# Kernel optimization log

Measured on AMD Instinct MI355X. Metric: run time of the kernel, lower is better.

## Reference

```python
import jax, jax.numpy as jnp
import numpy as np

EMBED_DIM = 1024
HEADS = 16
HEAD_DIM = EMBED_DIM // HEADS


def setup_inputs() -> dict:
    key = jax.random.key(0)
    ks = jax.random.split(key, 9)
    D = EMBED_DIM
    s = 1.0 / np.sqrt(D)
    x = jax.random.normal(ks[0], (4, 2048, D), dtype=jnp.float32)
    Wq = jax.random.uniform(ks[1], (D, D), jnp.float32, -s, s)
    bq = jnp.zeros((D,), jnp.float32)
    Wk = jax.random.uniform(ks[2], (D, D), jnp.float32, -s, s)
    bk = jnp.zeros((D,), jnp.float32)
    Wv = jax.random.uniform(ks[3], (D, D), jnp.float32, -s, s)
    bv = jnp.zeros((D,), jnp.float32)
    Wo = jax.random.uniform(ks[4], (D, D), jnp.float32, -s, s)
    bo = jnp.zeros((D,), jnp.float32)
    gamma = jnp.ones((D,), jnp.float32)
    beta = jnp.zeros((D,), jnp.float32)
    return {"x": x, "Wq": Wq, "bq": bq, "Wk": Wk, "bk": bk,
            "Wv": Wv, "bv": bv, "Wo": Wo, "bo": bo,
            "gamma": gamma, "beta": beta}


def reference(x, Wq, bq, Wk, bk, Wv, bv, Wo, bo, gamma, beta):
    B, S, D = x.shape
    H, Dh = HEADS, HEAD_DIM
    # projections -> [B, H, S, Dh]
    q = (x @ Wq + bq).reshape(B, S, H, Dh).transpose(0, 2, 1, 3)
    k = (x @ Wk + bk).reshape(B, S, H, Dh).transpose(0, 2, 1, 3)
    v = (x @ Wv + bv).reshape(B, S, H, Dh).transpose(0, 2, 1, 3)
    scores = jnp.einsum('bhqd,bhkd->bhqk', q, k) / jnp.sqrt(jnp.float32(Dh))
    attn = jax.nn.softmax(scores, axis=-1)  # dropout is identity in eval
    ctx = jnp.einsum('bhqk,bhkd->bhqd', attn, v)
    ctx = ctx.transpose(0, 2, 1, 3).reshape(B, S, D)
    out = ctx @ Wo + bo
    # residual + LayerNorm (eps=1e-5, torch default)
    h = out + x
    mu = jnp.mean(h, axis=-1, keepdims=True)
    var = jnp.mean(jnp.square(h - mu), axis=-1, keepdims=True)
    return (h - mu) * jax.lax.rsqrt(var + 1e-5) * gamma + beta
```

## Files before the change

kernel.cpp:

```cpp
#include <hip/hip_runtime.h>
#include <hip/hip_bf16.h>
#include <stdint.h>

typedef short sh4 __attribute__((ext_vector_type(4)));
typedef short sh8 __attribute__((ext_vector_type(8)));
typedef float fl4 __attribute__((ext_vector_type(4)));
typedef float f32x4 __attribute__((ext_vector_type(4)));
typedef float f32x16 __attribute__((ext_vector_type(16)));
typedef uint32_t u32x4 __attribute__((ext_vector_type(4)));

static __device__ __forceinline__ short f2bf(float f) {
  union { float f; uint32_t u; } v;
  v.f = f;
  uint32_t r = v.u + 0x7fffu + ((v.u >> 16) & 1u);
  return (short)(r >> 16);
}

static __device__ __forceinline__ uint32_t cvt_pk_bf16(float a, float b) {
  uint32_t r;
  asm("v_cvt_pk_bf16_f32 %0, %1, %2" : "=v"(r) : "v"(a), "v"(b));
  return r;
}

static __device__ __forceinline__ void pl32swap(uint32_t& a, uint32_t& b) {
  asm volatile("v_permlane32_swap_b32 %0, %1" : "+v"(a), "+v"(b));
}

static __device__ __forceinline__ void gload_lds16(const void* g, void* l) {
  __builtin_amdgcn_global_load_lds((const __attribute__((address_space(1))) void*)g,
                                   (__attribute__((address_space(3))) void*)l, 16, 0, 0);
}

__global__ __launch_bounds__(256) void k_wt(const float* __restrict__ Wq, const float* __restrict__ Wk,
                                            const float* __restrict__ Wv, const float* __restrict__ Wo,
                                            short* __restrict__ Tq, short* __restrict__ Tk,
                                            short* __restrict__ Tv, short* __restrict__ To) {
  const float* W = blockIdx.z == 0 ? Wq : blockIdx.z == 1 ? Wk : blockIdx.z == 2 ? Wv : Wo;
  short* T = blockIdx.z == 0 ? Tq : blockIdx.z == 1 ? Tk : blockIdx.z == 2 ? Tv : To;
  __shared__ float tile[32][33];
  int n0 = blockIdx.x * 32, k0 = blockIdx.y * 32;
  int tx = threadIdx.x, ty = threadIdx.y;
#pragma unroll
  for (int p = 0; p < 4; p++) tile[ty + 8 * p][tx] = W[(size_t)(k0 + ty + 8 * p) * 1024 + n0 + tx];
  __syncthreads();
#pragma unroll
  for (int p = 0; p < 4; p++) T[(size_t)(n0 + ty + 8 * p) * 1024 + k0 + tx] = f2bf(tile[tx][ty + 8 * p]);
}

__global__ __launch_bounds__(256) void k_cvtx(const float* __restrict__ x, short* __restrict__ o) {
  int i = blockIdx.x * 256 + threadIdx.x;
  fl4 v = ((const fl4*)x)[i];
  sh4 r;
#pragma unroll
  for (int j = 0; j < 4; j++) r[j] = f2bf(v[j]);
  ((sh4*)o)[i] = r;
}

#define GEMM_PIPE_LOOP(STAGE_BODY, COMPUTE_BODY)                         \
  STAGE_BODY(0, 0);                                                      \
  STAGE_BODY(1, 1);                                                      \
  {                                                                      \
    int bufc = 0, bufs = 2;                                              \
    for (int it = 0; it < 32; it++) {                                    \
      if (it < 31)                                                       \
        asm volatile("s_waitcnt vmcnt(4)" ::: "memory");                 \
      else                                                               \
        asm volatile("s_waitcnt vmcnt(0)" ::: "memory");                 \
      __builtin_amdgcn_s_barrier();                                      \
      if (it + 2 < 32) { STAGE_BODY(it + 2, bufs); }                     \
      __builtin_amdgcn_sched_barrier(0);                                 \
      { int buf = bufc; COMPUTE_BODY }                                   \
      bufc = bufc == 2 ? 0 : bufc + 1;                                   \
      bufs = bufs == 2 ? 0 : bufs + 1;                                   \
      asm volatile("" ::: "memory");                                     \
    }                                                                    \
  }

__global__ __launch_bounds__(256) void k_qk(const short* __restrict__ A, const short* __restrict__ WT2,
                                            const float* __restrict__ bq, const float* __restrict__ bk,
                                            short* __restrict__ Qo, short* __restrict__ Ko, float qscale) {
  __shared__ __align__(16) short As[3][128 * 32];
  __shared__ __align__(16) short Bs[3][128 * 32];
  const int xcd = blockIdx.x & 7, j = blockIdx.x >> 3;
  const int m0 = (xcd + 8 * (j & 7)) * 128, n0 = (j >> 3) * 128;
  const int sec = n0 >> 10;
  const float* bias = sec == 0 ? bq : bk;
  short* Out = sec == 0 ? Qo : Ko;
  const float scale = sec == 0 ? qscale : 1.f;
  const int t = threadIdx.x;
  const int lane = t & 63, w = t >> 6;
  const int wr = w >> 1, wc = w & 1;
  const int l15 = lane & 15, g = lane >> 4;
  f32x4 acc[4][4];
#pragma unroll
  for (int mi = 0; mi < 4; mi++)
#pragma unroll
    for (int ni = 0; ni < 4; ni++) acc[mi][ni] = (f32x4){0.f, 0.f, 0.f, 0.f};

#define QK_STAGE(kt, buf)                                                                     \
  {                                                                                           \
    int r0 = w * 32;                                                                          \
    _Pragma("unroll") for (int i = 0; i < 2; i++) {                                           \
      int row = r0 + i * 16 + (lane >> 2);                                                    \
      gload_lds16(&A[(size_t)(m0 + row) * 1024 + (kt) * 32 + (lane & 3) * 8],                 \
                  &As[buf][(r0 + i * 16) * 32]);                                              \
      gload_lds16(&WT2[(size_t)(n0 + row) * 1024 + (kt) * 32 + (lane & 3) * 8],               \
                  &Bs[buf][(r0 + i * 16) * 32]);                                              \
    }                                                                                         \
  }

#define QK_COMPUTE                                                                            \
  sh8 a[4], b[4];                                                                             \
  _Pragma("unroll") for (int i = 0; i < 4; i++)                                               \
      a[i] = *(sh8*)&As[buf][(wr * 64 + i * 16 + l15) * 32 + g * 8];                          \
  _Pragma("unroll") for (int i = 0; i < 4; i++)                                               \
      b[i] = *(sh8*)&Bs[buf][(wc * 64 + i * 16 + l15) * 32 + g * 8];                          \
  _Pragma("unroll") for (int mi = 0; mi < 4; mi++)                                            \
      _Pragma("unroll") for (int ni = 0; ni < 4; ni++)                                        \
          acc[mi][ni] = __builtin_amdgcn_mfma_f32_16x16x32_bf16(b[ni], a[mi], acc[mi][ni], 0, 0, 0);

  GEMM_PIPE_LOOP(QK_STAGE, QK_COMPUTE)

#pragma unroll
  for (int ni = 0; ni < 4; ni++) {
    int nbase = n0 + wc * 64 + ni * 16 + g * 4;
    int nn0 = nbase & 1023;
    fl4 bv4 = *(const fl4*)&bias[nn0];
    int h = nn0 >> 6, dh0 = nn0 & 63;
#pragma unroll
    for (int mi = 0; mi < 4; mi++) {
      int m = m0 + wr * 64 + mi * 16 + l15;
      int bb = m >> 11, s = m & 2047;
      uint2 dd;
      dd.x = cvt_pk_bf16((acc[mi][ni][0] + bv4[0]) * scale, (acc[mi][ni][1] + bv4[1]) * scale);
      dd.y = cvt_pk_bf16((acc[mi][ni][2] + bv4[2]) * scale, (acc[mi][ni][3] + bv4[3]) * scale);
      *(uint2*)&Out[(((size_t)bb * 16 + h) * 2048 + s) * 64 + dh0] = dd;
    }
  }
}

__global__ __launch_bounds__(256) void k_v(const short* __restrict__ A, const short* __restrict__ WTv,
                                           const float* __restrict__ bv, short* __restrict__ Vo) {
  __shared__ __align__(16) short As[3][128 * 32];
  __shared__ __align__(16) short Bs[3][128 * 32];
  const int xcd = blockIdx.x & 7, j = blockIdx.x >> 3;
  const int m0 = (xcd + 8 * (j & 7)) * 128, n0 = (j >> 3) * 128;
  const int t = threadIdx.x;
  const int lane = t & 63, w = t >> 6;
  const int wr = w >> 1, wc = w & 1;
  const int l15 = lane & 15, g = lane >> 4;
  f32x4 acc[4][4];
#pragma unroll
  for (int mi = 0; mi < 4; mi++)
#pragma unroll
    for (int ni = 0; ni < 4; ni++) acc[mi][ni] = (f32x4){0.f, 0.f, 0.f, 0.f};

#define V_STAGE(kt, buf)                                                                      \
  {                                                                                           \
    int r0 = w * 32;                                                                          \
    _Pragma("unroll") for (int i = 0; i < 2; i++) {                                           \
      int row = r0 + i * 16 + (lane >> 2);                                                    \
      gload_lds16(&A[(size_t)(m0 + row) * 1024 + (kt) * 32 + (lane & 3) * 8],                 \
                  &As[buf][(r0 + i * 16) * 32]);                                              \
      gload_lds16(&WTv[(size_t)(n0 + row) * 1024 + (kt) * 32 + (lane & 3) * 8],               \
                  &Bs[buf][(r0 + i * 16) * 32]);                                              \
    }                                                                                         \
  }

#define V_COMPUTE                                                                             \
  sh8 a[4], b[4];                                                                             \
  _Pragma("unroll") for (int i = 0; i < 4; i++)                                               \
      a[i] = *(sh8*)&As[buf][(wr * 64 + i * 16 + l15) * 32 + g * 8];                          \
  _Pragma("unroll") for (int i = 0; i < 4; i++)                                               \
      b[i] = *(sh8*)&Bs[buf][(wc * 64 + i * 16 + l15) * 32 + g * 8];                          \
  _Pragma("unroll") for (int mi = 0; mi < 4; mi++)                                            \
      _Pragma("unroll") for (int ni = 0; ni < 4; ni++)                                        \
          acc[mi][ni] = __builtin_amdgcn_mfma_f32_16x16x32_bf16(a[mi], b[ni], acc[mi][ni], 0, 0, 0);

  GEMM_PIPE_LOOP(V_STAGE, V_COMPUTE)

#pragma unroll
  for (int ni = 0; ni < 4; ni++) {
    int col = n0 + wc * 64 + ni * 16 + l15;
    int nn = col & 1023;
    float bvv = bv[nn];
    int h = nn >> 6, dh = nn & 63;
#pragma unroll
    for (int mi = 0; mi < 4; mi++) {
      int mr = m0 + wr * 64 + mi * 16 + g * 4;
      int bb = mr >> 11, s = mr & 2047;
      uint2 dd;
      dd.x = cvt_pk_bf16(acc[mi][ni][0] + bvv, acc[mi][ni][1] + bvv);
      dd.y = cvt_pk_bf16(acc[mi][ni][2] + bvv, acc[mi][ni][3] + bvv);
      *(uint2*)&Vo[(((size_t)bb * 16 + h) * 64 + dh) * 2048 + s] = dd;
    }
  }
}

__global__ __launch_bounds__(256) void k_oproj(const short* __restrict__ A, const short* __restrict__ BT,
                                               const float* __restrict__ bias, const float* __restrict__ X,
                                               float* __restrict__ Out) {
  __shared__ __align__(16) short As[3][128 * 32];
  __shared__ __align__(16) short Bs[3][128 * 32];
  const int xcd = blockIdx.x & 7, j = blockIdx.x >> 3;
  const int m0 = (xcd + 8 * (j & 7)) * 128, n0 = (j >> 3) * 128;
  const int t = threadIdx.x;
  const int lane = t & 63, w = t >> 6;
  const int wr = w >> 1, wc = w & 1;
  const int l15 = lane & 15, g = lane >> 4;
  f32x4 acc[4][4];
#pragma unroll
  for (int mi = 0; mi < 4; mi++)
#pragma unroll
    for (int ni = 0; ni < 4; ni++) acc[mi][ni] = (f32x4){0.f, 0.f, 0.f, 0.f};

#define O_STAGE(kt, buf)                                                                      \
  {                                                                                           \
    int r0 = w * 32;                                                                          \
    _Pragma("unroll") for (int i = 0; i < 2; i++) {                                           \
      int row = r0 + i * 16 + (lane >> 2);                                                    \
      gload_lds16(&A[(size_t)(m0 + row) * 1024 + (kt) * 32 + (lane & 3) * 8],                 \
                  &As[buf][(r0 + i * 16) * 32]);                                              \
      gload_lds16(&BT[(size_t)(n0 + row) * 1024 + (kt) * 32 + (lane & 3) * 8],                \
                  &Bs[buf][(r0 + i * 16) * 32]);                                              \
    }                                                                                         \
  }

#define O_COMPUTE                                                                             \
  sh8 a[4], b[4];                                                                             \
  _Pragma("unroll") for (int i = 0; i < 4; i++)                                               \
      a[i] = *(sh8*)&As[buf][(wr * 64 + i * 16 + l15) * 32 + g * 8];                          \
  _Pragma("unroll") for (int i = 0; i < 4; i++)                                               \
      b[i] = *(sh8*)&Bs[buf][(wc * 64 + i * 16 + l15) * 32 + g * 8];                          \
  _Pragma("unroll") for (int mi = 0; mi < 4; mi++)                                            \
      _Pragma("unroll") for (int ni = 0; ni < 4; ni++)                                        \
          acc[mi][ni] = __builtin_amdgcn_mfma_f32_16x16x32_bf16(b[ni], a[mi], acc[mi][ni], 0, 0, 0);

  GEMM_PIPE_LOOP(O_STAGE, O_COMPUTE)

#pragma unroll
  for (int ni = 0; ni < 4; ni++) {
    int nbase = n0 + wc * 64 + ni * 16 + g * 4;
    fl4 bv4 = *(const fl4*)&bias[nbase];
#pragma unroll
    for (int mi = 0; mi < 4; mi++) {
      int m = m0 + wr * 64 + mi * 16 + l15;
      fl4 xv = *(const fl4*)&X[(size_t)m * 1024 + nbase];
      fl4 r;
#pragma unroll
      for (int e = 0; e < 4; e++) r[e] = acc[mi][ni][e] + bv4[e] + xv[e];
      *(fl4*)&Out[(size_t)m * 1024 + nbase] = r;
    }
  }
}

__global__ __launch_bounds__(512, 4) void k_attn(const short* __restrict__ Q, const short* __restrict__ K,
                                                 const short* __restrict__ Vt, short* __restrict__ CTX) {
  const int nid = (blockIdx.x & 7) * 64 + (blockIdx.x >> 3);
  const int qbi = nid & 7, h = (nid >> 3) & 15, b = nid >> 7;
  const int q0 = qbi * 256;
  const size_t ho = (((size_t)b * 16 + h) * 2048) * 64;
  const short* Qh = Q + ho;
  const short* Kh = K + ho;
  const short* Vh = Vt + ho;
  __shared__ __align__(16) short Ks[3][8 * 512];
  __shared__ __align__(16) short Vs[4][8 * 512];
  const int t = threadIdx.x, lane = t & 63, w = t >> 6;
  const int l31 = lane & 31, hi = lane >> 5;

  sh8 qreg[4];
#pragma unroll
  for (int ks = 0; ks < 4; ks++)
    qreg[ks] = *(const sh8*)&Qh[(size_t)(q0 + w * 32 + l31) * 64 + ks * 16 + hi * 8];

  f32x16 zinit;
#pragma unroll
  for (int r = 0; r < 16; r++) zinit[r] = 0.f;

  f32x16 oc0 = zinit, oc1 = zinit;
  float l_s = 0.f;
  u32x4 pwp[4];

  auto stageK = [&](int kt, int buf) {
    gload_lds16(&Kh[(size_t)(kt * 64 + (w >> 2) * 32 + l31) * 64 + (w & 3) * 16 + hi * 8],
                (char*)&Ks[buf][0] + w * 1024);
  };
  auto stageV = [&](int kt, int buf) {
    gload_lds16(&Vh[(size_t)((w >> 2) * 32 + l31) * 2048 + kt * 64 + (w & 3) * 16 + hi * 8],
                (char*)&Vs[buf][0] + w * 1024);
  };

  stageK(0, 0); stageV(0, 0);
  stageK(1, 1); stageV(1, 1);

  for (int kt = 0; kt < 32; kt++) {
    if (kt < 31)
      asm volatile("s_waitcnt vmcnt(2)" ::: "memory");
    else
      asm volatile("s_waitcnt vmcnt(0)" ::: "memory");
    __builtin_amdgcn_s_barrier();
    if (kt + 2 < 32) { stageK(kt + 2, (kt + 2) % 3); stageV(kt + 2, (kt + 2) & 3); }
    __builtin_amdgcn_sched_barrier(0);
    const int kbuf = kt % 3;

    f32x16 s0, s1;
    __builtin_amdgcn_s_setprio(1);
#pragma unroll
    for (int ks = 0; ks < 4; ks++) {
      sh8 ak0 = *(sh8*)((char*)&Ks[kbuf][0] + ks * 1024 + lane * 16);
      sh8 ak1 = *(sh8*)((char*)&Ks[kbuf][0] + (4 + ks) * 1024 + lane * 16);
      if (ks == 0) {
        s0 = __builtin_amdgcn_mfma_f32_32x32x16_bf16(ak0, qreg[0], zinit, 0, 0, 0);
        s1 = __builtin_amdgcn_mfma_f32_32x32x16_bf16(ak1, qreg[0], zinit, 0, 0, 0);
      } else {
        s0 = __builtin_amdgcn_mfma_f32_32x32x16_bf16(ak0, qreg[ks], s0, 0, 0, 0);
        s1 = __builtin_amdgcn_mfma_f32_32x32x16_bf16(ak1, qreg[ks], s1, 0, 0, 0);
      }
    }

    if (kt > 0) {
      const int vb = (kt - 1) & 3;
#pragma unroll
      for (int ks = 0; ks < 4; ks++) {
        sh8 pb = __builtin_bit_cast(sh8, pwp[ks]);
        sh8 av0 = *(sh8*)((char*)&Vs[vb][0] + ks * 1024 + lane * 16);
        sh8 av1 = *(sh8*)((char*)&Vs[vb][0] + (4 + ks) * 1024 + lane * 16);
        oc0 = __builtin_amdgcn_mfma_f32_32x32x16_bf16(av0, pb, oc0, 0, 0, 0);
        oc1 = __builtin_amdgcn_mfma_f32_32x32x16_bf16(av1, pb, oc1, 0, 0, 0);
      }
    }
    __builtin_amdgcn_s_setprio(0);

    float ps = 0.f;
#pragma unroll
    for (int r = 0; r < 16; r++) { s0[r] = __builtin_amdgcn_exp2f(s0[r]); ps += s0[r]; }
#pragma unroll
    for (int r = 0; r < 16; r++) { s1[r] = __builtin_amdgcn_exp2f(s1[r]); ps += s1[r]; }
    l_s += ps;

    {
      uint32_t a0 = cvt_pk_bf16(s0[0], s0[1]), a1 = cvt_pk_bf16(s0[2], s0[3]);
      uint32_t b0 = cvt_pk_bf16(s0[4], s0[5]), b1 = cvt_pk_bf16(s0[6], s0[7]);
      uint32_t c0 = cvt_pk_bf16(s0[8], s0[9]), c1 = cvt_pk_bf16(s0[10], s0[11]);
      uint32_t d0 = cvt_pk_bf16(s0[12], s0[13]), d1 = cvt_pk_bf16(s0[14], s0[15]);
      pl32swap(a0, b0); pl32swap(a1, b1); pl32swap(c0, d0); pl32swap(c1, d1);
      pwp[0] = (u32x4){a0, a1, b0, b1};
      pwp[1] = (u32x4){c0, c1, d0, d1};
      a0 = cvt_pk_bf16(s1[0], s1[1]); a1 = cvt_pk_bf16(s1[2], s1[3]);
      b0 = cvt_pk_bf16(s1[4], s1[5]); b1 = cvt_pk_bf16(s1[6], s1[7]);
      c0 = cvt_pk_bf16(s1[8], s1[9]); c1 = cvt_pk_bf16(s1[10], s1[11]);
      d0 = cvt_pk_bf16(s1[12], s1[13]); d1 = cvt_pk_bf16(s1[14], s1[15]);
      pl32swap(a0, b0); pl32swap(a1, b1); pl32swap(c0, d0); pl32swap(c1, d1);
      pwp[2] = (u32x4){a0, a1, b0, b1};
      pwp[3] = (u32x4){c0, c1, d0, d1};
    }
    asm volatile("" ::: "memory");
  }

  {
    const int vb = 31 & 3;
    __builtin_amdgcn_s_setprio(1);
#pragma unroll
    for (int ks = 0; ks < 4; ks++) {
      sh8 pb = __builtin_bit_cast(sh8, pwp[ks]);
      sh8 av0 = *(sh8*)((char*)&Vs[vb][0] + ks * 1024 + lane * 16);
      sh8 av1 = *(sh8*)((char*)&Vs[vb][0] + (4 + ks) * 1024 + lane * 16);
      oc0 = __builtin_amdgcn_mfma_f32_32x32x16_bf16(av0, pb, oc0, 0, 0, 0);
      oc1 = __builtin_amdgcn_mfma_f32_32x32x16_bf16(av1, pb, oc1, 0, 0, 0);
    }
    __builtin_amdgcn_s_setprio(0);
  }

  l_s += __shfl_xor(l_s, 32);
  float li = 1.f / l_s;
  int s = q0 + w * 32 + l31;
  size_t obase = (((size_t)b * 2048 + s) * 16 + h) * 64;
#pragma unroll
  for (int rq = 0; rq < 4; rq++) {
    uint2 dd;
    dd.x = cvt_pk_bf16(oc0[4 * rq] * li, oc0[4 * rq + 1] * li);
    dd.y = cvt_pk_bf16(oc0[4 * rq + 2] * li, oc0[4 * rq + 3] * li);
    *(uint2*)&CTX[obase + rq * 8 + hi * 4] = dd;
    dd.x = cvt_pk_bf16(oc1[4 * rq] * li, oc1[4 * rq + 1] * li);
    dd.y = cvt_pk_bf16(oc1[4 * rq + 2] * li, oc1[4 * rq + 3] * li);
    *(uint2*)&CTX[obase + 32 + rq * 8 + hi * 4] = dd;
  }
}

__global__ __launch_bounds__(256) void k_ln(float* __restrict__ Out, const float* __restrict__ gamma,
                                            const float* __restrict__ beta) {
  int row = blockIdx.x * 4 + (threadIdx.x >> 6);
  int lane = threadIdx.x & 63;
  float* p = Out + (size_t)row * 1024;
  fl4 v[4];
  float s = 0.f, s2 = 0.f;
#pragma unroll
  for (int j = 0; j < 4; j++) {
    v[j] = *(fl4*)&p[lane * 4 + j * 256];
#pragma unroll
    for (int e = 0; e < 4; e++) { s += v[j][e]; s2 += v[j][e] * v[j][e]; }
  }
#pragma unroll
  for (int off = 1; off < 64; off <<= 1) {
    s += __shfl_xor(s, off);
    s2 += __shfl_xor(s2, off);
  }
  float mu = s * (1.f / 1024.f);
  float var = s2 * (1.f / 1024.f) - mu * mu;
  float inv = rsqrtf(var + 1e-5f);
#pragma unroll
  for (int j = 0; j < 4; j++) {
    fl4 r;
#pragma unroll
    for (int e = 0; e < 4; e++) {
      int c = lane * 4 + j * 256 + e;
      r[e] = (v[j][e] - mu) * inv * gamma[c] + beta[c];
    }
    *(fl4*)&p[lane * 4 + j * 256] = r;
  }
}

extern "C" void kernel_launch(void* const* d_in, const int* in_sizes, int n_in,
                              void* d_out, int out_size, void* d_ws, size_t ws_size,
                              hipStream_t stream) {
  (void)in_sizes; (void)n_in; (void)out_size; (void)ws_size;
  const float* x = (const float*)d_in[0];
  const float* Wq = (const float*)d_in[1];
  const float* bq = (const float*)d_in[2];
  const float* Wk = (const float*)d_in[3];
  const float* bk = (const float*)d_in[4];
  const float* Wv = (const float*)d_in[5];
  const float* bv = (const float*)d_in[6];
  const float* Wo = (const float*)d_in[7];
  const float* bo = (const float*)d_in[8];
  const float* gamma = (const float*)d_in[9];
  const float* beta = (const float*)d_in[10];
  float* out = (float*)d_out;
  char* ws = (char*)d_ws;
  short* xbf = (short*)(ws);
  short* wtq = (short*)(ws + (16ull << 20));
  short* wtk = (short*)(ws + (18ull << 20));
  short* wtv = (short*)(ws + (20ull << 20));
  short* wto = (short*)(ws + (22ull << 20));
  short* qb  = (short*)(ws + (24ull << 20));
  short* kbuf = (short*)(ws + (40ull << 20));
  short* vbuf = (short*)(ws + (56ull << 20));
  short* ctx = (short*)(ws + (72ull << 20));

  const float QSCALE = 0.125f * 1.44269504088896f;

  k_wt<<<dim3(32, 32, 4), dim3(32, 8), 0, stream>>>(Wq, Wk, Wv, Wo, wtq, wtk, wtv, wto);
  k_cvtx<<<8192, 256, 0, stream>>>(x, xbf);
  k_qk<<<1024, 256, 0, stream>>>(xbf, wtq, bq, bk, qb, kbuf, QSCALE);
  k_v<<<512, 256, 0, stream>>>(xbf, wtv, bv, vbuf);
  k_attn<<<512, 512, 0, stream>>>(qb, kbuf, vbuf, ctx);
  k_oproj<<<512, 256, 0, stream>>>(ctx, wto, bo, x, out);
  k_ln<<<2048, 256, 0, stream>>>(out, gamma, beta);
}
```

Measured before the change: 212.9 us.

## Switch projection GEMMs to 32x32x16 MFMA with fragment-ordered LDS layout and new tiling

All three projection GEMMs (QK, V, O) move from 16x16x32 to 32x32x16 bf16 MFMA. Global-to-LDS loads are rearranged so each 1KB LDS chunk already holds one MFMA operand fragment, letting each lane read its fragment with a single contiguous 16-byte load. The QK kernel grows to 256x128 tiles with 512 threads, and the block-to-tile mappings are reassigned so blocks on the same XCD share weight columns for L2 reuse. The intent is fewer LDS instructions and bank conflicts per MFMA and better cache locality, at the cost of higher register pressure from the larger accumulators and changed occupancy hints.

```diff
diff --git a/kernel.cpp b/kernel.cpp
--- a/kernel.cpp
+++ b/kernel.cpp
@@ -56,14 +56,14 @@
   ((sh4*)o)[i] = r;
 }
 
-#define GEMM_PIPE_LOOP(STAGE_BODY, COMPUTE_BODY)                         \
+#define PIPE_LOOP(STAGE_BODY, COMPUTE_BODY, VM)                          \
   STAGE_BODY(0, 0);                                                      \
   STAGE_BODY(1, 1);                                                      \
   {                                                                      \
     int bufc = 0, bufs = 2;                                              \
     for (int it = 0; it < 32; it++) {                                    \
       if (it < 31)                                                       \
-        asm volatile("s_waitcnt vmcnt(4)" ::: "memory");                 \
+        asm volatile("s_waitcnt vmcnt(" VM ")" ::: "memory");            \
       else                                                               \
         asm volatile("s_waitcnt vmcnt(0)" ::: "memory");                 \
       __builtin_amdgcn_s_barrier();                                      \
@@ -76,13 +76,13 @@
     }                                                                    \
   }
 
-__global__ __launch_bounds__(256) void k_qk(const short* __restrict__ A, const short* __restrict__ WT2,
-                                            const float* __restrict__ bq, const float* __restrict__ bk,
-                                            short* __restrict__ Qo, short* __restrict__ Ko, float qscale) {
-  __shared__ __align__(16) short As[3][128 * 32];
-  __shared__ __align__(16) short Bs[3][128 * 32];
+__global__ __launch_bounds__(512, 4) void k_qk(const short* __restrict__ A, const short* __restrict__ WT2,
+                                               const float* __restrict__ bq, const float* __restrict__ bk,
+                                               short* __restrict__ Qo, short* __restrict__ Ko, float qscale) {
+  __shared__ __align__(16) short As[3][8192];
+  __shared__ __align__(16) short Bs[3][4096];
   const int xcd = blockIdx.x & 7, j = blockIdx.x >> 3;
-  const int m0 = (xcd + 8 * (j & 7)) * 128, n0 = (j >> 3) * 128;
+  const int m0 = (j >> 1) * 256, n0 = (xcd * 2 + (j & 1)) * 128;
   const int sec = n0 >> 10;
   const float* bias = sec == 0 ? bq : bk;
   short* Out = sec == 0 ? Qo : Ko;
@@ -90,166 +90,186 @@
   const int t = threadIdx.x;
   const int lane = t & 63, w = t >> 6;
   const int wr = w >> 1, wc = w & 1;
-  const int l15 = lane & 15, g = lane >> 4;
-  f32x4 acc[4][4];
-#pragma unroll
-  for (int mi = 0; mi < 4; mi++)
-#pragma unroll
-    for (int ni = 0; ni < 4; ni++) acc[mi][ni] = (f32x4){0.f, 0.f, 0.f, 0.f};
+  const int l31 = lane & 31, hi = lane >> 5;
+  f32x16 acc[2][2];
+#pragma unroll
+  for (int mi = 0; mi < 2; mi++)
+#pragma unroll
+    for (int ni = 0; ni < 2; ni++)
+#pragma unroll
+      for (int r = 0; r < 16; r++) acc[mi][ni][r] = 0.f;
 
 #define QK_STAGE(kt, buf)                                                                     \
   {                                                                                           \
-    int r0 = w * 32;                                                                          \
-    _Pragma("unroll") for (int i = 0; i < 2; i++) {                                           \
-      int row = r0 + i * 16 + (lane >> 2);                                                    \
-      gload_lds16(&A[(size_t)(m0 + row) * 1024 + (kt) * 32 + (lane & 3) * 8],                 \
-                  &As[buf][(r0 + i * 16) * 32]);                                              \
-      gload_lds16(&WT2[(size_t)(n0 + row) * 1024 + (kt) * 32 + (lane & 3) * 8],               \
-                  &Bs[buf][(r0 + i * 16) * 32]);                                              \
-    }                                                                                         \
+    _Pragma("unroll") for (int i = 0; i < 2; i++)                                             \
+        gload_lds16(&A[(size_t)(m0 + w * 32 + l31) * 1024 + (kt) * 32 + i * 16 + hi * 8],     \
+                    (char*)&As[buf][0] + (w * 2 + i) * 1024);                                 \
+    gload_lds16(&WT2[(size_t)(n0 + (w >> 1) * 32 + l31) * 1024 + (kt) * 32 + (w & 1) * 16 + hi * 8], \
+                (char*)&Bs[buf][0] + w * 1024);                                               \
   }
 
 #define QK_COMPUTE                                                                            \
-  sh8 a[4], b[4];                                                                             \
-  _Pragma("unroll") for (int i = 0; i < 4; i++)                                               \
-      a[i] = *(sh8*)&As[buf][(wr * 64 + i * 16 + l15) * 32 + g * 8];                          \
-  _Pragma("unroll") for (int i = 0; i < 4; i++)                                               \
-      b[i] = *(sh8*)&Bs[buf][(wc * 64 + i * 16 + l15) * 32 + g * 8];                          \
-  _Pragma("unroll") for (int mi = 0; mi < 4; mi++)                                            \
-      _Pragma("unroll") for (int ni = 0; ni < 4; ni++)                                        \
-          acc[mi][ni] = __builtin_amdgcn_mfma_f32_16x16x32_bf16(b[ni], a[mi], acc[mi][ni], 0, 0, 0);
-
-  GEMM_PIPE_LOOP(QK_STAGE, QK_COMPUTE)
-
-#pragma unroll
-  for (int ni = 0; ni < 4; ni++) {
-    int nbase = n0 + wc * 64 + ni * 16 + g * 4;
-    int nn0 = nbase & 1023;
-    fl4 bv4 = *(const fl4*)&bias[nn0];
-    int h = nn0 >> 6, dh0 = nn0 & 63;
-#pragma unroll
-    for (int mi = 0; mi < 4; mi++) {
-      int m = m0 + wr * 64 + mi * 16 + l15;
-      int bb = m >> 11, s = m & 2047;
-      uint2 dd;
-      dd.x = cvt_pk_bf16((acc[mi][ni][0] + bv4[0]) * scale, (acc[mi][ni][1] + bv4[1]) * scale);
-      dd.y = cvt_pk_bf16((acc[mi][ni][2] + bv4[2]) * scale, (acc[mi][ni][3] + bv4[3]) * scale);
-      *(uint2*)&Out[(((size_t)bb * 16 + h) * 2048 + s) * 64 + dh0] = dd;
-    }
-  }
-}
-
-__global__ __launch_bounds__(256) void k_v(const short* __restrict__ A, const short* __restrict__ WTv,
-                                           const float* __restrict__ bv, short* __restrict__ Vo) {
-  __shared__ __align__(16) short As[3][128 * 32];
-  __shared__ __align__(16) short Bs[3][128 * 32];
+  _Pragma("unroll") for (int ks = 0; ks < 2; ks++) {                                          \
+    sh8 a0 = *(sh8*)((char*)&As[buf][0] + ((2 * wr + 0) * 2 + ks) * 1024 + lane * 16);        \
+    sh8 a1 = *(sh8*)((char*)&As[buf][0] + ((2 * wr + 1) * 2 + ks) * 1024 + lane * 16);        \
+    sh8 b0 = *(sh8*)((char*)&Bs[buf][0] + ((2 * wc + 0) * 2 + ks) * 1024 + lane * 16);        \
+    sh8 b1 = *(sh8*)((char*)&Bs[buf][0] + ((2 * wc + 1) * 2 + ks) * 1024 + lane * 16);        \
+    acc[0][0] = __builtin_amdgcn_mfma_f32_32x32x16_bf16(b0, a0, acc[0][0], 0, 0, 0);          \
+    acc[0][1] = __builtin_amdgcn_mfma_f32_32x32x16_bf16(b1, a0, acc[0][1], 0, 0, 0);          \
+    acc[1][0] = __builtin_amdgcn_mfma_f32_32x32x16_bf16(b0, a1, acc[1][0], 0, 0, 0);          \
+    acc[1][1] = __builtin_amdgcn_mfma_f32_32x32x16_bf16(b1, a1, acc[1][1], 0, 0, 0);          \
+  }
+
+  PIPE_LOOP(QK_STAGE, QK_COMPUTE, "3")
+
+#pragma unroll
+  for (int mi = 0; mi < 2; mi++) {
+    int m = m0 + (2 * wr + mi) * 32 + l31;
+    int bb = m >> 11, s = m & 2047;
+#pragma unroll
+    for (int ni = 0; ni < 2; ni++) {
+      int nbase0 = n0 + (2 * wc + ni) * 32;
+#pragma unroll
+      for (int rq = 0; rq < 4; rq++) {
+        int n_lo = nbase0 + 8 * rq + 4 * hi;
+        int nn = n_lo & 1023;
+        fl4 bv4 = *(const fl4*)&bias[nn];
+        int h = nn >> 6, dh0 = nn & 63;
+        uint2 dd;
+        dd.x = cvt_pk_bf16((acc[mi][ni][4 * rq] + bv4[0]) * scale,
+                           (acc[mi][ni][4 * rq + 1] + bv4[1]) * scale);
+        dd.y = cvt_pk_bf16((acc[mi][ni][4 * rq + 2] + bv4[2]) * scale,
+                           (acc[mi][ni][4 * rq + 3] + bv4[3]) * scale);
+        *(uint2*)&Out[(((size_t)bb * 16 + h) * 2048 + s) * 64 + dh0] = dd;
+      }
+    }
+  }
+}
+
+__global__ __launch_bounds__(256, 3) void k_v(const short* __restrict__ A, const short* __restrict__ WTv,
+                                              const float* __restrict__ bv, short* __restrict__ Vo) {
+  __shared__ __align__(16) short As[3][4096];
+  __shared__ __align__(16) short Bs[3][4096];
   const int xcd = blockIdx.x & 7, j = blockIdx.x >> 3;
-  const int m0 = (xcd + 8 * (j & 7)) * 128, n0 = (j >> 3) * 128;
+  const int m0 = j * 128, n0 = xcd * 128;
   const int t = threadIdx.x;
   const int lane = t & 63, w = t >> 6;
   const int wr = w >> 1, wc = w & 1;
-  const int l15 = lane & 15, g = lane >> 4;
-  f32x4 acc[4][4];
-#pragma unroll
-  for (int mi = 0; mi < 4; mi++)
-#pragma unroll
-    for (int ni = 0; ni < 4; ni++) acc[mi][ni] = (f32x4){0.f, 0.f, 0.f, 0.f};
+  const int l31 = lane & 31, hi = lane >> 5;
+  f32x16 acc[2][2];
+#pragma unroll
+  for (int mi = 0; mi < 2; mi++)
+#pragma unroll
+    for (int ni = 0; ni < 2; ni++)
+#pragma unroll
+      for (int r = 0; r < 16; r++) acc[mi][ni][r] = 0.f;
 
 #define V_STAGE(kt, buf)                                                                      \
   {                                                                                           \
-    int r0 = w * 32;                                                                          \
     _Pragma("unroll") for (int i = 0; i < 2; i++) {                                           \
-      int row = r0 + i * 16 + (lane >> 2);                                                    \
-      gload_lds16(&A[(size_t)(m0 + row) * 1024 + (kt) * 32 + (lane & 3) * 8],                 \
-                  &As[buf][(r0 + i * 16) * 32]);                                              \
-      gload_lds16(&WTv[(size_t)(n0 + row) * 1024 + (kt) * 32 + (lane & 3) * 8],               \
-                  &Bs[buf][(r0 + i * 16) * 32]);                                              \
+      int c = 2 * w + i;                                                                      \
+      gload_lds16(&A[(size_t)(m0 + (c >> 1) * 32 + l31) * 1024 + (kt) * 32 + (c & 1) * 16 + hi * 8], \
+                  (char*)&As[buf][0] + c * 1024);                                             \
+      gload_lds16(&WTv[(size_t)(n0 + (c >> 1) * 32 + l31) * 1024 + (kt) * 32 + (c & 1) * 16 + hi * 8], \
+                  (char*)&Bs[buf][0] + c * 1024);                                             \
     }                                                                                         \
   }
 
 #define V_COMPUTE                                                                             \
-  sh8 a[4], b[4];                                                                             \
-  _Pragma("unroll") for (int i = 0; i < 4; i++)                                               \
-      a[i] = *(sh8*)&As[buf][(wr * 64 + i * 16 + l15) * 32 + g * 8];                          \
-  _Pragma("unroll") for (int i = 0; i < 4; i++)                                               \
-      b[i] = *(sh8*)&Bs[buf][(wc * 64 + i * 16 + l15) * 32 + g * 8];                          \
-  _Pragma("unroll") for (int mi = 0; mi < 4; mi++)                                            \
-      _Pragma("unroll") for (int ni = 0; ni < 4; ni++)                                        \
-          acc[mi][ni] = __builtin_amdgcn_mfma_f32_16x16x32_bf16(a[mi], b[ni], acc[mi][ni], 0, 0, 0);
-
-  GEMM_PIPE_LOOP(V_STAGE, V_COMPUTE)
-
-#pragma unroll
-  for (int ni = 0; ni < 4; ni++) {
-    int col = n0 + wc * 64 + ni * 16 + l15;
-    int nn = col & 1023;
-    float bvv = bv[nn];
-    int h = nn >> 6, dh = nn & 63;
-#pragma unroll
-    for (int mi = 0; mi < 4; mi++) {
-      int mr = m0 + wr * 64 + mi * 16 + g * 4;
-      int bb = mr >> 11, s = mr & 2047;
-      uint2 dd;
-      dd.x = cvt_pk_bf16(acc[mi][ni][0] + bvv, acc[mi][ni][1] + bvv);
-      dd.y = cvt_pk_bf16(acc[mi][ni][2] + bvv, acc[mi][ni][3] + bvv);
-      *(uint2*)&Vo[(((size_t)bb * 16 + h) * 64 + dh) * 2048 + s] = dd;
-    }
-  }
-}
-
-__global__ __launch_bounds__(256) void k_oproj(const short* __restrict__ A, const short* __restrict__ BT,
-                                               const float* __restrict__ bias, const float* __restrict__ X,
-                                               float* __restrict__ Out) {
-  __shared__ __align__(16) short As[3][128 * 32];
-  __shared__ __align__(16) short Bs[3][128 * 32];
+  _Pragma("unroll") for (int ks = 0; ks < 2; ks++) {                                          \
+    sh8 a0 = *(sh8*)((char*)&As[buf][0] + ((2 * wr + 0) * 2 + ks) * 1024 + lane * 16);        \
+    sh8 a1 = *(sh8*)((char*)&As[buf][0] + ((2 * wr + 1) * 2 + ks) * 1024 + lane * 16);        \
+    sh8 b0 = *(sh8*)((char*)&Bs[buf][0] + ((2 * wc + 0) * 2 + ks) * 1024 + lane * 16);        \
+    sh8 b1 = *(sh8*)((char*)&Bs[buf][0] + ((2 * wc + 1) * 2 + ks) * 1024 + lane * 16);        \
+    acc[0][0] = __builtin_amdgcn_mfma_f32_32x32x16_bf16(a0, b0, acc[0][0], 0, 0, 0);          \
+    acc[0][1] = __builtin_amdgcn_mfma_f32_32x32x16_bf16(a0, b1, acc[0][1], 0, 0, 0);          \
+    acc[1][0] = __builtin_amdgcn_mfma_f32_32x32x16_bf16(a1, b0, acc[1][0], 0, 0, 0);          \
+    acc[1][1] = __builtin_amdgcn_mfma_f32_32x32x16_bf16(a1, b1, acc[1][1], 0, 0, 0);          \
+  }
+
+  PIPE_LOOP(V_STAGE, V_COMPUTE, "4")
+
+#pragma unroll
+  for (int ni = 0; ni < 2; ni++) {
+    int col = n0 + (2 * wc + ni) * 32 + l31;
+    int h = col >> 6, dh = col & 63;
+    float bvv = bv[col];
+#pragma unroll
+    for (int mi = 0; mi < 2; mi++) {
+      int mbase = m0 + (2 * wr + mi) * 32;
+#pragma unroll
+      for (int rq = 0; rq < 4; rq++) {
+        int s_lo = mbase + 8 * rq + 4 * hi;
+        int bb = s_lo >> 11, s = s_lo & 2047;
+        uint2 dd;
+        dd.x = cvt_pk_bf16(acc[mi][ni][4 * rq] + bvv, acc[mi][ni][4 * rq + 1] + bvv);
+        dd.y = cvt_pk_bf16(acc[mi][ni][4 * rq + 2] + bvv, acc[mi][ni][4 * rq + 3] + bvv);
+        *(uint2*)&Vo[(((size_t)bb * 16 + h) * 64 + dh) * 2048 + s] = dd;
+      }
+    }
+  }
+}
+
+__global__ __launch_bounds__(256, 3) void k_oproj(const short* __restrict__ A, const short* __restrict__ BT,
+                                                  const float* __restrict__ bias, const float* __restrict__ X,
+                                                  float* __restrict__ Out) {
+  __shared__ __align__(16) short As[3][4096];
+  __shared__ __align__(16) short Bs[3][4096];
   const int xcd = blockIdx.x & 7, j = blockIdx.x >> 3;
-  const int m0 = (xcd + 8 * (j & 7)) * 128, n0 = (j >> 3) * 128;
+  const int m0 = j * 128, n0 = xcd * 128;
   const int t = threadIdx.x;
   const int lane = t & 63, w = t >> 6;
   const int wr = w >> 1, wc = w & 1;
-  const int l15 = lane & 15, g = lane >> 4;
-  f32x4 acc[4][4];
-#pragma unroll
-  for (int mi = 0; mi < 4; mi++)
-#pragma unroll
-    for (int ni = 0; ni < 4; ni++) acc[mi][ni] = (f32x4){0.f, 0.f, 0.f, 0.f};
+  const int l31 = lane & 31, hi = lane >> 5;
+  f32x16 acc[2][2];
+#pragma unroll
+  for (int mi = 0; mi < 2; mi++)
+#pragma unroll
+    for (int ni = 0; ni < 2; ni++)
+#pragma unroll
+      for (int r = 0; r < 16; r++) acc[mi][ni][r] = 0.f;
 
 #define O_STAGE(kt, buf)                                                                      \
   {                                                                                           \
-    int r0 = w * 32;                                                                          \
     _Pragma("unroll") for (int i = 0; i < 2; i++) {                                           \
-      int row = r0 + i * 16 + (lane >> 2);                                                    \
-      gload_lds16(&A[(size_t)(m0 + row) * 1024 + (kt) * 32 + (lane & 3) * 8],                 \
-                  &As[buf][(r0 + i * 16) * 32]);                                              \
-      gload_lds16(&BT[(size_t)(n0 + row) * 1024 + (kt) * 32 + (lane & 3) * 8],                \
-                  &Bs[buf][(r0 + i * 16) * 32]);                                              \
+      int c = 2 * w + i;                                                                      \
+      gload_lds16(&A[(size_t)(m0 + (c >> 1) * 32 + l31) * 1024 + (kt) * 32 + (c & 1) * 16 + hi * 8], \
+                  (char*)&As[buf][0] + c * 1024);                                             \
+      gload_lds16(&BT[(size_t)(n0 + (c >> 1) * 32 + l31) * 1024 + (kt) * 32 + (c & 1) * 16 + hi * 8], \
+                  (char*)&Bs[buf][0] + c * 1024);                                             \
     }                                                                                         \
   }
 
 #define O_COMPUTE                                                                             \
-  sh8 a[4], b[4];                                                                             \
-  _Pragma("unroll") for (int i = 0; i < 4; i++)                                               \
-      a[i] = *(sh8*)&As[buf][(wr * 64 + i * 16 + l15) * 32 + g * 8];                          \
-  _Pragma("unroll") for (int i = 0; i < 4; i++)                                               \
-      b[i] = *(sh8*)&Bs[buf][(wc * 64 + i * 16 + l15) * 32 + g * 8];                          \
-  _Pragma("unroll") for (int mi = 0; mi < 4; mi++)                                            \
-      _Pragma("unroll") for (int ni = 0; ni < 4; ni++)                                        \
-          acc[mi][ni] = __builtin_amdgcn_mfma_f32_16x16x32_bf16(b[ni], a[mi], acc[mi][ni], 0, 0, 0);
-
-  GEMM_PIPE_LOOP(O_STAGE, O_COMPUTE)
-
-#pragma unroll
-  for (int ni = 0; ni < 4; ni++) {
-    int nbase = n0 + wc * 64 + ni * 16 + g * 4;
-    fl4 bv4 = *(const fl4*)&bias[nbase];
-#pragma unroll
-    for (int mi = 0; mi < 4; mi++) {
-      int m = m0 + wr * 64 + mi * 16 + l15;
-      fl4 xv = *(const fl4*)&X[(size_t)m * 1024 + nbase];
-      fl4 r;
-#pragma unroll
-      for (int e = 0; e < 4; e++) r[e] = acc[mi][ni][e] + bv4[e] + xv[e];
-      *(fl4*)&Out[(size_t)m * 1024 + nbase] = r;
+  _Pragma("unroll") for (int ks = 0; ks < 2; ks++) {                                          \
+    sh8 a0 = *(sh8*)((char*)&As[buf][0] + ((2 * wr + 0) * 2 + ks) * 1024 + lane * 16);        \
+    sh8 a1 = *(sh8*)((char*)&As[buf][0] + ((2 * wr + 1) * 2 + ks) * 1024 + lane * 16);        \
+    sh8 b0 = *(sh8*)((char*)&Bs[buf][0] + ((2 * wc + 0) * 2 + ks) * 1024 + lane * 16);        \
+    sh8 b1 = *(sh8*)((char*)&Bs[buf][0] + ((2 * wc + 1) * 2 + ks) * 1024 + lane * 16);        \
+    acc[0][0] = __builtin_amdgcn_mfma_f32_32x32x16_bf16(b0, a0, acc[0][0], 0, 0, 0);          \
+    acc[0][1] = __builtin_amdgcn_mfma_f32_32x32x16_bf16(b1, a0, acc[0][1], 0, 0, 0);          \
+    acc[1][0] = __builtin_amdgcn_mfma_f32_32x32x16_bf16(b0, a1, acc[1][0], 0, 0, 0);          \
+    acc[1][1] = __builtin_amdgcn_mfma_f32_32x32x16_bf16(b1, a1, acc[1][1], 0, 0, 0);          \
+  }
+
+  PIPE_LOOP(O_STAGE, O_COMPUTE, "4")
+
+#pragma unroll
+  for (int mi = 0; mi < 2; mi++) {
+    int m = m0 + (2 * wr + mi) * 32 + l31;
+#pragma unroll
+    for (int ni = 0; ni < 2; ni++) {
+      int nbase0 = n0 + (2 * wc + ni) * 32;
+#pragma unroll
+      for (int rq = 0; rq < 4; rq++) {
+        int n_lo = nbase0 + 8 * rq + 4 * hi;
+        fl4 bv4 = *(const fl4*)&bias[n_lo];
+        fl4 xv = *(const fl4*)&X[(size_t)m * 1024 + n_lo];
+        fl4 r;
+#pragma unroll
+        for (int e = 0; e < 4; e++) r[e] = acc[mi][ni][4 * rq + e] + bv4[e] + xv[e];
+        *(fl4*)&Out[(size_t)m * 1024 + n_lo] = r;
+      }
     }
   }
 }
@@ -451,7 +471,7 @@
 
   k_wt<<<dim3(32, 32, 4), dim3(32, 8), 0, stream>>>(Wq, Wk, Wv, Wo, wtq, wtk, wtv, wto);
   k_cvtx<<<8192, 256, 0, stream>>>(x, xbf);
-  k_qk<<<1024, 256, 0, stream>>>(xbf, wtq, bq, bk, qb, kbuf, QSCALE);
+  k_qk<<<512, 512, 0, stream>>>(xbf, wtq, bq, bk, qb, kbuf, QSCALE);
   k_v<<<512, 256, 0, stream>>>(xbf, wtv, bv, vbuf);
   k_attn<<<512, 512, 0, stream>>>(qb, kbuf, vbuf, ctx);
   k_oproj<<<512, 256, 0, stream>>>(ctx, wto, bo, x, out);
```

New measurement: 248.3 us. +16.7%, slower.
